# Kernel tuning notes

Measured on AMD Instinct MI355X. Metric: run time of the kernel, lower is better.

## Reference

```python
import jax, jax.numpy as jnp
import numpy as np

B = 262144
HIDDEN = 128      # eqx.nn.MLP width_size
NUM_CODES = 512
EMBED_DIM = 256


def setup_inputs() -> dict:
    key = jax.random.key(0)
    ks = jax.random.split(key, 8)
    return {
        "x": jax.random.normal(ks[0], (B, 1), dtype=jnp.float32),
        "enc_w1": jax.random.normal(ks[1], (HIDDEN, 1), dtype=jnp.float32) * 0.5,
        "enc_b1": jax.random.normal(ks[2], (HIDDEN,), dtype=jnp.float32) * 0.1,
        "enc_w2": jax.random.normal(ks[3], (NUM_CODES, HIDDEN), dtype=jnp.float32) * 0.08,
        "enc_b2": jax.random.normal(ks[4], (NUM_CODES,), dtype=jnp.float32) * 0.1,
        "emb": jax.random.normal(ks[5], (NUM_CODES, EMBED_DIM), dtype=jnp.float32) * 0.1,
        "dec_w": jax.random.normal(ks[6], (1, EMBED_DIM), dtype=jnp.float32) * 0.06,
        "dec_b": jax.random.normal(ks[7], (1,), dtype=jnp.float32) * 0.1,
    }


def reference(x, enc_w1, enc_b1, enc_w2, enc_b2, emb, dec_w, dec_b):
    # encoder MLP: Linear(1,128) -> relu -> Linear(128,num_codes)
    h = jax.nn.relu(jnp.einsum("bi,hi->bh", x, enc_w1) + enc_b1)      # [B,128]
    logits = jnp.einsum("bh,ch->bc", h, enc_w2) + enc_b2               # [B,C]
    soft_probs = jax.nn.softmax(logits, axis=-1)                       # [B,C]
    hard_idx = jnp.argmax(logits, axis=-1)                             # [B]
    hard_probs = jax.nn.one_hot(hard_idx, NUM_CODES, dtype=soft_probs.dtype)
    ste_probs = soft_probs + jax.lax.stop_gradient(hard_probs - soft_probs)
    z = jnp.einsum("bc,cd->bd", ste_probs, emb)                        # [B,D]
    out = jnp.einsum("bd,od->bo", z, dec_w) + dec_b                    # [B,1]
    return out, hard_idx
```

## Files before the change

kernel.cpp:

```cpp
#include <hip/hip_runtime.h>


#define B_SAMPLES 262144
#define HIDDEN    128
#define NUM_CODES 512
#define EMBED_DIM 256
#define NUM_INT   129


__device__ __forceinline__ int classify(const double* ts, double xv) {
  int lo = 0, hi = HIDDEN;
  while (lo < hi) { int mid = (lo + hi) >> 1; if (ts[mid] > xv) hi = mid; else lo = mid + 1; }
  return lo;
}

__global__ void __launch_bounds__(512) k_build(
    const float* __restrict__ w1, const float* __restrict__ b1,
    const float* __restrict__ w2, const float* __restrict__ b2,
    const float* __restrict__ emb, const float* __restrict__ decw,
    const float* __restrict__ decb, double* __restrict__ t_sorted,
    double* __restrict__ code_out, int* __restrict__ env_cnt,
    double* __restrict__ env_xs, int* __restrict__ env_idx) {
  const int blk = blockIdx.x, tid = threadIdx.x;
  if (blk >= NUM_INT) {
    __shared__ double sdw[EMBED_DIM];
    if (tid < EMBED_DIM) sdw[tid] = (double)decw[tid];
    __syncthreads();
    if (tid < 256) {
      const int c = (blk - NUM_INT) * 256 + tid;
      const float4* e4 = (const float4*)(emb + c * EMBED_DIM);
      double s = 0.0;
#pragma unroll 8
      for (int q = 0; q < EMBED_DIM / 4; ++q) {
        const float4 v = e4[q];
        const int j = q * 4;
        s = fma((double)v.x, sdw[j + 0], s);
        s = fma((double)v.y, sdw[j + 1], s);
        s = fma((double)v.z, sdw[j + 2], s);
        s = fma((double)v.w, sdw[j + 3], s);
      }
      code_out[c] = s + (double)decb[0];
    }
    return;
  }
  __shared__ double tloc[HIDDEN], ts[HIDDEN], wj[HIDDEN], bj[HIDDEN];
  __shared__ double2 sAB[NUM_CODES];
  const int i = blk;
  if (tid < HIDDEN) {
    const double w = (double)w1[tid], b = (double)b1[tid];
    double t = -b / w;
    if (!isfinite(t)) t = 1e30;
    t = fmin(fmax(t, -1e30), 1e30);
    tloc[tid] = t;
  }
  __syncthreads();
  if (tid < HIDDEN) {
    const double t = tloc[tid];
    int r = 0;
    for (int k = 0; k < HIDDEN; ++k) {
      const double tk = tloc[k];
      r += (tk < t) || (tk == t && k < tid);
    }
    ts[r] = t;
  }
  __syncthreads();
  if (i == 0 && tid < HIDDEN) t_sorted[tid] = ts[tid];
  double xm;
  if (i == 0)           xm = ts[0] - 1.0;
  else if (i == HIDDEN) xm = ts[HIDDEN - 1] + 1.0;
  else                  xm = 0.5 * (ts[i - 1] + ts[i]);
  if (tid < HIDDEN) {
    const double w = (double)w1[tid], b = (double)b1[tid];
    const bool act = fma(w, xm, b) > 0.0;
    wj[tid] = act ? w : 0.0;
    bj[tid] = act ? b : 0.0;
  }
  __syncthreads();
  {
    const int c = tid;
    const float4* r4 = (const float4*)(w2 + c * HIDDEN);
    double A = 0.0, Bv = 0.0;
#pragma unroll 8
    for (int q = 0; q < HIDDEN / 4; ++q) {
      const float4 v = r4[q];
      const int j = q * 4;
      A  = fma((double)v.x, wj[j + 0], A);
      A  = fma((double)v.y, wj[j + 1], A);
      A  = fma((double)v.z, wj[j + 2], A);
      A  = fma((double)v.w, wj[j + 3], A);
      Bv = fma((double)v.x, bj[j + 0], Bv);
      Bv = fma((double)v.y, bj[j + 1], Bv);
      Bv = fma((double)v.z, bj[j + 2], Bv);
      Bv = fma((double)v.w, bj[j + 3], Bv);
    }
    sAB[c] = make_double2(A, Bv + (double)b2[c]);
  }
  __syncthreads();
  if (tid >= 64) return;
  const int lane = tid;
  double LA[8], LB[8];
#pragma unroll
  for (int j = 0; j < 8; ++j) {
    const double2 ab = sAB[lane + 64 * j];
    LA[j] = ab.x;
    LB[j] = ab.y;
  }
  const bool has_lo = (i > 0), has_hi = (i < HIDDEN);
  const double xlo = ts[has_lo ? i - 1 : 0];
  const double xhi = ts[has_hi ? i : 0];

  double bA = LA[0], bB = LB[0];
  int bc = lane;
  if (!has_lo) {
#pragma unroll
    for (int j = 1; j < 8; ++j) {
      const bool t = (LA[j] < bA) || (LA[j] == bA && LB[j] > bB);
      if (t) { bA = LA[j]; bB = LB[j]; bc = lane + 64 * j; }
    }
#pragma unroll
    for (int s = 32; s; s >>= 1) {
      const double oA = __shfl_xor(bA, s), oB = __shfl_xor(bB, s);
      const int oc = __shfl_xor(bc, s);
      const bool t = (oA < bA) || (oA == bA && (oB > bB || (oB == bB && oc < bc)));
      if (t) { bA = oA; bB = oB; bc = oc; }
    }
  } else {
#pragma unroll
    for (int j = 1; j < 8; ++j) {
      const double sg = fma(LA[j] - bA, xlo, LB[j] - bB);
      const bool t = (sg > 0.0) || (sg == 0.0 && LA[j] > bA);
      if (t) { bA = LA[j]; bB = LB[j]; bc = lane + 64 * j; }
    }
#pragma unroll
    for (int s = 32; s; s >>= 1) {
      const double oA = __shfl_xor(bA, s), oB = __shfl_xor(bB, s);
      const int oc = __shfl_xor(bc, s);
      const double sg = fma(oA - bA, xlo, oB - bB);
      const bool t = (sg > 0.0) || (sg == 0.0 && (oA > bA || (oA == bA && oc < bc)));
      if (t) { bA = oA; bB = oB; bc = oc; }
    }
  }
  bc = __shfl(bc, 0);
  double2 cur = sAB[bc];
  double Ac = cur.x, Bc = cur.y;
  const int base = i << 9;
  if (lane == 0) { env_xs[base] = -1e300; env_idx[base] = bc; }
  int r = 1;

  while (r < NUM_CODES) {
    double bn = 1.0, bd = 0.0, bA2 = 0.0;
    int bc2 = -1;
#pragma unroll
    for (int j = 0; j < 8; ++j) {
      const double d = LA[j] - Ac;
      const double n = Bc - LB[j];
      const double l = n * bd, rr = bn * d;
      const bool t = (d > 0.0) &&
                     ((l < rr) || (l == rr && bd != 0.0 && LA[j] > bA2));
      if (t) { bn = n; bd = d; bA2 = LA[j]; bc2 = lane + 64 * j; }
    }
#pragma unroll
    for (int s = 32; s; s >>= 1) {
      const double on = __shfl_xor(bn, s), od = __shfl_xor(bd, s);
      const double oA = __shfl_xor(bA2, s);
      const int oc = __shfl_xor(bc2, s);
      bool t;
      if (bd == 0.0) t = (od != 0.0);
      else if (od == 0.0) t = false;
      else {
        const double l = on * bd, rr = bn * od;
        t = (l < rr) || (l == rr && (oA > bA2 || (oA == bA2 && oc < bc2)));
      }
      if (t) { bn = on; bd = od; bA2 = oA; bc2 = oc; }
    }
    const int win = __shfl(bc2, 0);
    if (win < 0) break;
    const double2 ab = sAB[win];
    const double d = ab.x - Ac, n = Bc - ab.y;
    if (has_hi && n >= xhi * d) break;
    if (lane == 0) { env_xs[base + r] = n / d; env_idx[base + r] = win; }
    Ac = ab.x; Bc = ab.y;
    ++r;
  }
  if (lane == 0) env_cnt[i] = r;
}

__global__ void __launch_bounds__(256) k_map(const float* __restrict__ x,
                       const double* __restrict__ t_sorted,
                       const int* __restrict__ env_cnt,
                       const double* __restrict__ env_xs,
                       const int* __restrict__ env_idx,
                       const double* __restrict__ code_out,
                       float* __restrict__ out, float* __restrict__ idx_out) {
  __shared__ double ts[HIDDEN];
  __shared__ double sco[NUM_CODES];
  __shared__ int scnt[NUM_INT];
  const int tid = threadIdx.x;
  if (tid < HIDDEN) ts[tid] = t_sorted[tid];
  if (tid < NUM_INT) scnt[tid] = env_cnt[tid];
  for (int t = tid; t < NUM_CODES; t += 256) sco[t] = code_out[t];
  __syncthreads();
  const int s = blockIdx.x * 512 + tid * 2;
  const float2 xv2 = *(const float2*)(x + s);
  const float xs2[2] = {xv2.x, xv2.y};
  float o[2], id[2];
#pragma unroll
  for (int k = 0; k < 2; ++k) {
    const double xv = (double)xs2[k];
    const int i = classify(ts, xv);
    const int base = i << 9;
    int lo = 0, hi = scnt[i] - 1;
    while (lo < hi) {
      const int mid = (lo + hi + 1) >> 1;
      if (env_xs[base + mid] <= xv) lo = mid; else hi = mid - 1;
    }
    const int ci = env_idx[base + lo];
    o[k]  = (float)sco[ci];
    id[k] = (float)ci;
  }
  *(float2*)(out + s)     = make_float2(o[0], o[1]);
  *(float2*)(idx_out + s) = make_float2(id[0], id[1]);
}

extern "C" void kernel_launch(void* const* d_in, const int* in_sizes, int n_in,
                              void* d_out, int out_size, void* d_ws, size_t ws_size,
                              hipStream_t stream) {
  const float* x    = (const float*)d_in[0];
  const float* w1   = (const float*)d_in[1];
  const float* b1   = (const float*)d_in[2];
  const float* w2   = (const float*)d_in[3];
  const float* b2   = (const float*)d_in[4];
  const float* emb  = (const float*)d_in[5];
  const float* decw = (const float*)d_in[6];
  const float* decb = (const float*)d_in[7];

  char* ws = (char*)d_ws;
  double* t_sorted = (double*)(ws + 0);
  double* code_out = (double*)(ws + 2048);
  int*    env_cnt  = (int*)   (ws + 8192);
  double* env_xs   = (double*)(ws + 16384);
  int*    env_idx  = (int*)   (ws + 544768);

  float* out  = (float*)d_out;
  float* idxo = out + B_SAMPLES;

  k_build<<<NUM_INT + 2,      512, 0, stream>>>(w1, b1, w2, b2, emb, decw, decb,
                                                t_sorted, code_out, env_cnt,
                                                env_xs, env_idx);
  k_map  <<<B_SAMPLES / 512,  256, 0, stream>>>(x, t_sorted, env_cnt, env_xs,
                                                env_idx, code_out, out, idxo);
}
```

Baseline: 90.04 us.

## Split envelope construction across 8 waves per interval and add uniform grid lookup

The upper-envelope walk in k_build, which ran on a single wave per ReLU interval, is now split across 8 waves, each covering a subinterval. Results are staged in shared memory and written out as concatenated segments, so the serial hull walk per wave becomes shorter. A uniform 2048-cell grid over [-8,8] is also built to narrow the interval binary search in k_map. The cost is more shared memory per build block, a larger envelope stride, and some duplicated breakpoints at subinterval boundaries.

```diff
diff --git a/kernel.cpp b/kernel.cpp
--- a/kernel.cpp
+++ b/kernel.cpp
@@ -6,6 +6,9 @@
 #define NUM_CODES 512
 #define EMBED_DIM 256
 #define NUM_INT   129
+#define GRID_N    2048
+#define GRID_X0   (-8.0)
+#define GRID_INV  128.0
 
 
 __device__ __forceinline__ int classify(const double* ts, double xv) {
@@ -20,6 +23,7 @@
     const float* __restrict__ emb, const float* __restrict__ decw,
     const float* __restrict__ decb, double* __restrict__ t_sorted,
     double* __restrict__ code_out, int* __restrict__ env_cnt,
+    unsigned char* __restrict__ grid,
     double* __restrict__ env_xs, int* __restrict__ env_idx) {
   const int blk = blockIdx.x, tid = threadIdx.x;
   if (blk >= NUM_INT) {
@@ -45,6 +49,9 @@
   }
   __shared__ double tloc[HIDDEN], ts[HIDDEN], wj[HIDDEN], bj[HIDDEN];
   __shared__ double2 sAB[NUM_CODES];
+  __shared__ double sxs[8][NUM_CODES];
+  __shared__ unsigned short sid[8][NUM_CODES];
+  __shared__ int scnt8[8], soff8[8];
   const int i = blk;
   if (tid < HIDDEN) {
     const double w = (double)w1[tid], b = (double)b1[tid];
@@ -64,7 +71,13 @@
     ts[r] = t;
   }
   __syncthreads();
-  if (i == 0 && tid < HIDDEN) t_sorted[tid] = ts[tid];
+  if (i == 0) {
+    if (tid < HIDDEN) t_sorted[tid] = ts[tid];
+    for (int g = tid; g <= GRID_N; g += 512) {
+      const double xg = GRID_X0 + (double)g * (1.0 / GRID_INV);
+      grid[g] = (unsigned char)classify(ts, xg);
+    }
+  }
   double xm;
   if (i == 0)           xm = ts[0] - 1.0;
   else if (i == HIDDEN) xm = ts[HIDDEN - 1] + 1.0;
@@ -96,8 +109,7 @@
     sAB[c] = make_double2(A, Bv + (double)b2[c]);
   }
   __syncthreads();
-  if (tid >= 64) return;
-  const int lane = tid;
+  const int w = tid >> 6, lane = tid & 63;
   double LA[8], LB[8];
 #pragma unroll
   for (int j = 0; j < 8; ++j) {
@@ -105,13 +117,25 @@
     LA[j] = ab.x;
     LB[j] = ab.y;
   }
-  const bool has_lo = (i > 0), has_hi = (i < HIDDEN);
-  const double xlo = ts[has_lo ? i - 1 : 0];
-  const double xhi = ts[has_hi ? i : 0];
+  const double xlo = (i > 0)      ? ts[i - 1] : 0.0;
+  const double xhi = (i < HIDDEN) ? ts[i]     : 0.0;
+  bool neginf = false, hasr = true;
+  double cw = 0.0, xr = 0.0;
+  if (i == 0) {
+    if (w == 0) neginf = true; else cw = xhi - (double)(8 - w);
+    xr = xhi - (double)(7 - w);
+  } else if (i == HIDDEN) {
+    cw = xlo + (double)w;
+    if (w == 7) hasr = false; else xr = xlo + (double)(w + 1);
+  } else {
+    const double wd = (xhi - xlo) * 0.125;
+    cw = (w == 0) ? xlo : fma(wd, (double)w, xlo);
+    xr = (w == 7) ? xhi : fma(wd, (double)(w + 1), xlo);
+  }
 
   double bA = LA[0], bB = LB[0];
   int bc = lane;
-  if (!has_lo) {
+  if (neginf) {
 #pragma unroll
     for (int j = 1; j < 8; ++j) {
       const bool t = (LA[j] < bA) || (LA[j] == bA && LB[j] > bB);
@@ -127,7 +151,7 @@
   } else {
 #pragma unroll
     for (int j = 1; j < 8; ++j) {
-      const double sg = fma(LA[j] - bA, xlo, LB[j] - bB);
+      const double sg = fma(LA[j] - bA, cw, LB[j] - bB);
       const bool t = (sg > 0.0) || (sg == 0.0 && LA[j] > bA);
       if (t) { bA = LA[j]; bB = LB[j]; bc = lane + 64 * j; }
     }
@@ -135,7 +159,7 @@
     for (int s = 32; s; s >>= 1) {
       const double oA = __shfl_xor(bA, s), oB = __shfl_xor(bB, s);
       const int oc = __shfl_xor(bc, s);
-      const double sg = fma(oA - bA, xlo, oB - bB);
+      const double sg = fma(oA - bA, cw, oB - bB);
       const bool t = (sg > 0.0) || (sg == 0.0 && (oA > bA || (oA == bA && oc < bc)));
       if (t) { bA = oA; bB = oB; bc = oc; }
     }
@@ -143,8 +167,10 @@
   bc = __shfl(bc, 0);
   double2 cur = sAB[bc];
   double Ac = cur.x, Bc = cur.y;
-  const int base = i << 9;
-  if (lane == 0) { env_xs[base] = -1e300; env_idx[base] = bc; }
+  if (lane == 0) {
+    sxs[w][0] = (w == 0) ? -1e300 : cw;
+    sid[w][0] = (unsigned short)bc;
+  }
   int r = 1;
 
   while (r < NUM_CODES) {
@@ -177,17 +203,32 @@
     if (win < 0) break;
     const double2 ab = sAB[win];
     const double d = ab.x - Ac, n = Bc - ab.y;
-    if (has_hi && n >= xhi * d) break;
-    if (lane == 0) { env_xs[base + r] = n / d; env_idx[base + r] = win; }
+    if (hasr && n >= xr * d) break;
+    if (lane == 0) { sxs[w][r] = n / d; sid[w][r] = (unsigned short)win; }
     Ac = ab.x; Bc = ab.y;
     ++r;
   }
-  if (lane == 0) env_cnt[i] = r;
+  if (lane == 0) scnt8[w] = r;
+  __syncthreads();
+  if (tid == 0) {
+    int acc = 0;
+#pragma unroll
+    for (int q = 0; q < 8; ++q) { soff8[q] = acc; acc += scnt8[q]; }
+    env_cnt[i] = acc;
+  }
+  __syncthreads();
+  const int gbase = (i << 10) + soff8[w];
+  const int nw = scnt8[w];
+  for (int j = lane; j < nw; j += 64) {
+    env_xs [gbase + j] = sxs[w][j];
+    env_idx[gbase + j] = (int)sid[w][j];
+  }
 }
 
 __global__ void __launch_bounds__(256) k_map(const float* __restrict__ x,
                        const double* __restrict__ t_sorted,
                        const int* __restrict__ env_cnt,
+                       const unsigned char* __restrict__ grid,
                        const double* __restrict__ env_xs,
                        const int* __restrict__ env_idx,
                        const double* __restrict__ code_out,
@@ -195,10 +236,13 @@
   __shared__ double ts[HIDDEN];
   __shared__ double sco[NUM_CODES];
   __shared__ int scnt[NUM_INT];
+  __shared__ unsigned char sgrid[2052];
   const int tid = threadIdx.x;
   if (tid < HIDDEN) ts[tid] = t_sorted[tid];
   if (tid < NUM_INT) scnt[tid] = env_cnt[tid];
   for (int t = tid; t < NUM_CODES; t += 256) sco[t] = code_out[t];
+  for (int t = tid; t < 513; t += 256)
+    ((unsigned int*)sgrid)[t] = ((const unsigned int*)grid)[t];
   __syncthreads();
   const int s = blockIdx.x * 512 + tid * 2;
   const float2 xv2 = *(const float2*)(x + s);
@@ -207,14 +251,20 @@
 #pragma unroll
   for (int k = 0; k < 2; ++k) {
     const double xv = (double)xs2[k];
-    const int i = classify(ts, xv);
-    const int base = i << 9;
-    int lo = 0, hi = scnt[i] - 1;
-    while (lo < hi) {
-      const int mid = (lo + hi + 1) >> 1;
-      if (env_xs[base + mid] <= xv) lo = mid; else hi = mid - 1;
-    }
-    const int ci = env_idx[base + lo];
+    int lo, hi;
+    const double gf = (xv - GRID_X0) * GRID_INV;
+    if (gf < 0.0)                 { lo = 0;              hi = sgrid[0];     }
+    else if (gf >= (double)GRID_N){ lo = sgrid[GRID_N];  hi = HIDDEN;       }
+    else { const int g = (int)gf;   lo = sgrid[g];       hi = sgrid[g + 1]; }
+    while (lo < hi) { const int mid = (lo + hi) >> 1; if (ts[mid] > xv) hi = mid; else lo = mid + 1; }
+    const int ii = lo;
+    const int base = ii << 10;
+    int l2 = 0, h2 = scnt[ii] - 1;
+    while (l2 < h2) {
+      const int mid = (l2 + h2 + 1) >> 1;
+      if (env_xs[base + mid] <= xv) l2 = mid; else h2 = mid - 1;
+    }
+    const int ci = env_idx[base + l2];
     o[k]  = (float)sco[ci];
     id[k] = (float)ci;
   }
@@ -235,18 +285,20 @@
   const float* decb = (const float*)d_in[7];
 
   char* ws = (char*)d_ws;
-  double* t_sorted = (double*)(ws + 0);
-  double* code_out = (double*)(ws + 2048);
-  int*    env_cnt  = (int*)   (ws + 8192);
-  double* env_xs   = (double*)(ws + 16384);
-  int*    env_idx  = (int*)   (ws + 544768);
+  double*        t_sorted = (double*)       (ws + 0);
+  double*        code_out = (double*)       (ws + 2048);
+  int*           env_cnt  = (int*)          (ws + 8192);
+  unsigned char* grid     = (unsigned char*)(ws + 12288);
+  double*        env_xs   = (double*)       (ws + 16384);
+  int*           env_idx  = (int*)          (ws + 1073152);
 
   float* out  = (float*)d_out;
   float* idxo = out + B_SAMPLES;
 
-  k_build<<<NUM_INT + 2,      512, 0, stream>>>(w1, b1, w2, b2, emb, decw, decb,
-                                                t_sorted, code_out, env_cnt,
-                                                env_xs, env_idx);
-  k_map  <<<B_SAMPLES / 512,  256, 0, stream>>>(x, t_sorted, env_cnt, env_xs,
-                                                env_idx, code_out, out, idxo);
+  k_build<<<NUM_INT + 2,     512, 0, stream>>>(w1, b1, w2, b2, emb, decw, decb,
+                                               t_sorted, code_out, env_cnt,
+                                               grid, env_xs, env_idx);
+  k_map  <<<B_SAMPLES / 512, 256, 0, stream>>>(x, t_sorted, env_cnt, grid,
+                                               env_xs, env_idx, code_out,
+                                               out, idxo);
 }
```

Result: slower. 92.19 us (+2.4%).
